# Optimization experiments

Measured on AMD Instinct MI355X. Metric: run time of the kernel, lower is better.

Reference implementation:

```python
import jax, jax.numpy as jnp
import numpy as np


def _hard_sigmoid(x):
    # Keras ConvLSTM2D default recurrent_activation
    return jnp.clip(0.2 * x + 0.5, 0.0, 1.0)


def _conv_same(x, w):
    # x: [B,H,W,Cin], w: [kh,kw,Cin,Cout]
    return jax.lax.conv_general_dilated(
        x, w, window_strides=(1, 1), padding='SAME',
        dimension_numbers=('NHWC', 'HWIO', 'NHWC'))


def setup_inputs() -> dict:
    key = jax.random.key(0)
    ks = jax.random.split(key, 6)
    B, T, H, W, F = 16, 16, 64, 64, 64
    return {
        'inputs': jax.random.normal(ks[0], (B, T, H, W, 1), jnp.float32),  # only T is used
        'h0': jax.random.normal(ks[1], (B, H, W, F), jnp.float32),
        'c0': jax.random.normal(ks[2], (B, H, W, F), jnp.float32),
        'kernels': jax.random.normal(ks[3], (T, 3, 3, F, 4 * F), jnp.float32) * 0.05,
        'rec_kernels': jax.random.normal(ks[4], (T, 3, 3, F, 4 * F), jnp.float32) * 0.05,
        'bias': jnp.zeros((T, 4 * F), jnp.float32),
    }


def reference(inputs, h0, c0, kernels, rec_kernels, bias):
    # The layer feeds h back as the cell input each step, so the cell input x == h.
    # By linearity, conv(h, Wk) + conv(h, Uk) == conv(h, Wk + Uk); we fuse the two convs.
    # Gate order (Keras ConvLSTM2DCell): i, f, c, o.
    def step(carry, params):
        h, c = carry
        Wk, Uk, b = params  # [3,3,F,4F], [3,3,F,4F], [4F]
        z = _conv_same(h, Wk + Uk) + b  # [B,H,W,4F]
        zi, zf, zc, zo = jnp.split(z, 4, axis=-1)
        i = _hard_sigmoid(zi)
        f = _hard_sigmoid(zf)
        c_new = f * c + i * jnp.tanh(zc)
        o = _hard_sigmoid(zo)
        h_new = o * jnp.tanh(c_new)
        return (h_new, c_new), h_new

    (_, _), hs = jax.lax.scan(step, (h0, c0), (kernels, rec_kernels, bias))
    return jnp.moveaxis(hs, 0, 1)  # [B, T, H, W, F]
```

## Files before the change

### kernel.cpp

```cpp
#include <hip/hip_runtime.h>
#include <math.h>

typedef _Float16 f16;
typedef _Float16 f16x4 __attribute__((ext_vector_type(4)));
typedef _Float16 f16x8 __attribute__((ext_vector_type(8)));
typedef float f32x4 __attribute__((ext_vector_type(4)));

#define NB 16
#define NT 16
#define NH 64
#define NW 64
#define NF 64
#define NG 256
#define HWF ((size_t)NH * NW * NF)
#define OUT_BSTRIDE ((size_t)NT * HWF)
#define RS2 8448
#define ZS 258
#define WSTEP ((size_t)18432)

#define MFMA(a, b, c) __builtin_amdgcn_mfma_f32_16x16x32_f16((a), (b), (c), 0, 0, 0)

__device__ __forceinline__ void gload_lds16(const void* g, void* l) {
    __builtin_amdgcn_global_load_lds(
        (const __attribute__((address_space(1))) unsigned int*)(g),
        (__attribute__((address_space(3))) unsigned int*)(l), 16, 0, 0);
}

__device__ __forceinline__ float hsig(float x) {
    return fminf(fmaxf(0.2f * x + 0.5f, 0.0f), 1.0f);
}

__device__ __forceinline__ float ftanh(float x) {
    float t = __builtin_amdgcn_exp2f(x * 2.885390081777927f);
    return 1.0f - 2.0f * __builtin_amdgcn_rcpf(t + 1.0f);
}

__global__ void fuse_w_hi(const float* __restrict__ k, const float* __restrict__ rk,
                          f16* __restrict__ wf2) {
    int idx = blockIdx.x * 256 + threadIdx.x;
    if (idx >= NT * 9 * NG * 8) return;
    int g8   = idx & 7;
    int cout = (idx >> 3) & 255;
    int tt   = idx >> 11;
    int tap  = tt % 9;
    int t    = tt / 9;
    int kk = g8 >> 2, lg = g8 & 3;

    const float* ks = k  + (size_t)tt * NF * NG + cout;
    const float* rs = rk + (size_t)tt * NF * NG + cout;

    f16 hi8[8];
#pragma unroll
    for (int j = 0; j < 8; ++j) {
        int cin = kk * 32 + lg * 8 + j;
        hi8[j] = (f16)(ks[(size_t)cin * NG] + rs[(size_t)cin * NG]);
    }
    const int lane = lg * 16 + (cout & 15);
    size_t chunk = (size_t)t * WSTEP + (size_t)(tap * 2 + kk) * 1024 +
                   (size_t)(cout >> 4) * 64 + lane;
    *(f16x8*)&wf2[chunk * 8] = *(f16x8*)hi8;
}

__global__ void f32_to_f16(const float* __restrict__ src, f16* __restrict__ dst, int n4) {
    int i = blockIdx.x * 256 + threadIdx.x;
    if (i >= n4) return;
    float4 v = ((const float4*)src)[i];
    f16x4 o = { (f16)v.x, (f16)v.y, (f16)v.z, (f16)v.w };
    *(f16x4*)&dst[(size_t)i * 4] = o;
}

__global__ void __launch_bounds__(512, 4)
convlstm_mfma_step(const f16* __restrict__ h2in, f16* __restrict__ h2out,
                   f16* __restrict__ cbuf,
                   float* __restrict__ hout,
                   const f16* __restrict__ wt,
                   const float* __restrict__ bias)
{
    __shared__ __align__(16) unsigned char lds[67584];

    const int tid  = threadIdx.x;
    const int w    = tid >> 6;
    const int lane = tid & 63;

    const int id    = blockIdx.x;
    const int bb    = ((id & 7) << 1) + ((id >> 8) & 1);
    const int y0    = ((id >> 3) & 31) * 2;

    if (tid < 64) {
        int row = tid >> 4, side = (tid >> 3) & 1, j = tid & 7;
        *(f16x8*)&lds[row * RS2 + side * (65 * 128) + j * 16] = (f16x8)(_Float16)0.0f;
    }

    {
        const int r    = w >> 1;
        const int gy   = y0 - 1 + r;
        const int half = w & 1;
        const unsigned dbase = r * RS2 + 128 + half * 4096;
        if (gy >= 0 && gy < NH) {
            const unsigned char* gsrc = (const unsigned char*)h2in +
                ((((size_t)bb * NH + gy) * NW) << 7);
#pragma unroll
            for (int i = 0; i < 4; ++i) {
                const int xrel = half * 32 + i * 8 + (lane >> 3);
                const unsigned src = ((unsigned)xrel << 7) +
                    ((unsigned)((lane & 7) ^ ((xrel + 1) & 7)) << 4);
                gload_lds16(gsrc + src, (void*)&lds[dbase + i * 1024]);
            }
        } else {
            const f16x8 zf = (f16x8)(_Float16)0.0f;
#pragma unroll
            for (int i = 0; i < 4; ++i)
                *(f16x8*)&lds[dbase + i * 1024 + lane * 16] = zf;
        }
    }
    __syncthreads();

    const int wm = w >> 2;
    const int wn = w & 3;
    const int lm = lane & 15;
    const int lg = lane >> 4;

    f32x4 acc[4][4];
#pragma unroll
    for (int mf = 0; mf < 4; ++mf)
#pragma unroll
        for (int nf = 0; nf < 4; ++nf) acc[mf][nf] = (f32x4)0.0f;

    unsigned av[3][2];
#pragma unroll
    for (int d = 0; d < 3; ++d)
#pragma unroll
        for (int kk = 0; kk < 2; ++kk) {
            const int tx = lm + d;
            av[d][kk] = (unsigned)(tx * 128 +
                        (((kk * 4 + lg) ^ (tx & 7)) << 4));
        }

    const f16x8* wb = (const f16x8*)wt + (size_t)(wn * 4) * 64 + lane;

    f16x8 bh[4];
#pragma unroll
    for (int it = 0; it < 18; ++it) {
        const int tap = it >> 1, kk = it & 1;
#pragma unroll
        for (int nf = 0; nf < 4; ++nf)
            bh[nf] = wb[(size_t)it * 1024 + nf * 64];
        const int ty = tap / 3;
        const int d  = tap - ty * 3;
        const unsigned abase = (unsigned)((wm + ty) * RS2) + av[d][kk];
        __builtin_amdgcn_s_setprio(1);
#pragma unroll
        for (int mf = 0; mf < 4; ++mf) {
            const f16x8 ah = *(const f16x8*)&lds[abase + mf * 2048];
#pragma unroll
            for (int nf = 0; nf < 4; ++nf)
                acc[mf][nf] = MFMA(ah, bh[nf], acc[mf][nf]);
        }
        __builtin_amdgcn_s_setprio(0);
    }

    __syncthreads();

    float* zbuf = (float*)lds;
    const int f = tid & 63;
    const float bi = bias[f], bfv = bias[64 + f], bcv = bias[128 + f], bov = bias[192 + f];

#pragma unroll 1
    for (int half = 0; half < 2; ++half) {
        if (wm == half) {
#pragma unroll
            for (int mf = 0; mf < 4; ++mf)
#pragma unroll
                for (int nf = 0; nf < 4; ++nf)
#pragma unroll
                    for (int j = 0; j < 4; ++j)
                        zbuf[(mf * 16 + lg * 4 + j) * ZS + wn * 64 + nf * 16 + lm] =
                            acc[mf][nf][j];
        }
        __syncthreads();
        const int gy = y0 + half;
#pragma unroll 1
        for (int k2 = 0; k2 < 8; ++k2) {
            const int x = (tid >> 6) + k2 * 8;
            const float* zz = zbuf + x * ZS;
            float zi  = zz[f]       + bi;
            float zfv = zz[64 + f]  + bfv;
            float zc  = zz[128 + f] + bcv;
            float zo  = zz[192 + f] + bov;
            size_t goff = (((size_t)bb * NH + gy) * NW + x) * NF + f;
            float cp = (float)cbuf[goff];
            float ig = hsig(zi), fg = hsig(zfv), og = hsig(zo);
            float cn = fg * cp + ig * ftanh(zc);
            cbuf[goff] = (f16)cn;
            float hn = og * ftanh(cn);
            hout[(size_t)bb * OUT_BSTRIDE + (((size_t)gy * NW + x) * NF + f)] = hn;
            h2out[goff] = (f16)hn;
        }
        __syncthreads();
    }
}

extern "C" void kernel_launch(void* const* d_in, const int* in_sizes, int n_in,
                              void* d_out, int out_size, void* d_ws, size_t ws_size,
                              hipStream_t stream) {
    const float* h0    = (const float*)d_in[1];
    const float* c0    = (const float*)d_in[2];
    const float* kern  = (const float*)d_in[3];
    const float* rkern = (const float*)d_in[4];
    const float* bias  = (const float*)d_in[5];
    float* out = (float*)d_out;

    f16* wf2   = (f16*)d_ws;
    f16* h2a   = wf2 + (size_t)NT * WSTEP * 8;
    f16* h2b   = h2a + (size_t)NB * HWF;
    f16* cbuf  = h2b + (size_t)NB * HWF;

    const int n4 = (int)(NB * HWF / 4);
    fuse_w_hi<<<(NT * 9 * NG * 8 + 255) / 256, 256, 0, stream>>>(kern, rkern, wf2);
    f32_to_f16<<<(n4 + 255) / 256, 256, 0, stream>>>(h0, h2a, n4);
    f32_to_f16<<<(n4 + 255) / 256, 256, 0, stream>>>(c0, cbuf, n4);

    for (int t = 0; t < NT; ++t) {
        const f16* hin = (t & 1) ? h2b : h2a;
        f16* hnx       = (t & 1) ? h2a : h2b;
        convlstm_mfma_step<<<dim3(512), 512, 0, stream>>>(
            hin, hnx, cbuf,
            out + (size_t)t * HWF,
            wf2 + (size_t)t * WSTEP * 8,
            bias + t * NG);
    }
}
```

Before: 444.0 us.

## Permute weight columns so each wave holds all four gates, drop LDS epilogue

Reorders the fused weight layout so the four N-fragments a wave computes correspond to the i, f, c, o gates of the same 16 features. The LSTM gate math can then run directly on MFMA accumulators in registers, which removes the LDS staging of the z tile, the extra barriers and the shrunken-but-large shared buffer. The first weight fragment load is also hoisted above the h tile load to overlap latency. Global stores become less coalesced (16 features per row segment instead of 64), and the smaller LDS footprint may allow higher occupancy.

```diff
diff --git a/kernel.cpp b/kernel.cpp
--- a/kernel.cpp
+++ b/kernel.cpp
@@ -15,7 +15,6 @@
 #define HWF ((size_t)NH * NW * NF)
 #define OUT_BSTRIDE ((size_t)NT * HWF)
 #define RS2 8448
-#define ZS 258
 #define WSTEP ((size_t)18432)
 
 #define MFMA(a, b, c) __builtin_amdgcn_mfma_f32_16x16x32_f16((a), (b), (c), 0, 0, 0)
@@ -56,8 +55,9 @@
         hi8[j] = (f16)(ks[(size_t)cin * NG] + rs[(size_t)cin * NG]);
     }
     const int lane = lg * 16 + (cout & 15);
+    const int cb   = ((cout >> 4) & 3) * 4 + (cout >> 6);
     size_t chunk = (size_t)t * WSTEP + (size_t)(tap * 2 + kk) * 1024 +
-                   (size_t)(cout >> 4) * 64 + lane;
+                   (size_t)cb * 64 + lane;
     *(f16x8*)&wf2[chunk * 8] = *(f16x8*)hi8;
 }
 
@@ -76,15 +76,26 @@
                    const f16* __restrict__ wt,
                    const float* __restrict__ bias)
 {
-    __shared__ __align__(16) unsigned char lds[67584];
+    __shared__ __align__(16) unsigned char lds[4 * RS2];
 
     const int tid  = threadIdx.x;
     const int w    = tid >> 6;
     const int lane = tid & 63;
 
-    const int id    = blockIdx.x;
-    const int bb    = ((id & 7) << 1) + ((id >> 8) & 1);
-    const int y0    = ((id >> 3) & 31) * 2;
+    const int id = blockIdx.x;
+    const int bb = ((id & 7) << 1) + ((id >> 8) & 1);
+    const int y0 = ((id >> 3) & 31) * 2;
+
+    const int wm = w >> 2;
+    const int wn = w & 3;
+    const int lm = lane & 15;
+    const int lg = lane >> 4;
+
+    const f16x8* wb = (const f16x8*)wt + (size_t)(wn * 4) * 64 + lane;
+    f16x8 bh[4];
+#pragma unroll
+    for (int nf = 0; nf < 4; ++nf)
+        bh[nf] = wb[nf * 64];
 
     if (tid < 64) {
         int row = tid >> 4, side = (tid >> 3) & 1, j = tid & 7;
@@ -115,11 +126,6 @@
     }
     __syncthreads();
 
-    const int wm = w >> 2;
-    const int wn = w & 3;
-    const int lm = lane & 15;
-    const int lg = lane >> 4;
-
     f32x4 acc[4][4];
 #pragma unroll
     for (int mf = 0; mf < 4; ++mf)
@@ -136,15 +142,14 @@
                         (((kk * 4 + lg) ^ (tx & 7)) << 4));
         }
 
-    const f16x8* wb = (const f16x8*)wt + (size_t)(wn * 4) * 64 + lane;
-
-    f16x8 bh[4];
 #pragma unroll
     for (int it = 0; it < 18; ++it) {
+        if (it > 0) {
+#pragma unroll
+            for (int nf = 0; nf < 4; ++nf)
+                bh[nf] = wb[(size_t)it * 1024 + nf * 64];
+        }
         const int tap = it >> 1, kk = it & 1;
-#pragma unroll
-        for (int nf = 0; nf < 4; ++nf)
-            bh[nf] = wb[(size_t)it * 1024 + nf * 64];
         const int ty = tap / 3;
         const int d  = tap - ty * 3;
         const unsigned abase = (unsigned)((wm + ty) * RS2) + av[d][kk];
@@ -159,44 +164,31 @@
         __builtin_amdgcn_s_setprio(0);
     }
 
-    __syncthreads();
-
-    float* zbuf = (float*)lds;
-    const int f = tid & 63;
-    const float bi = bias[f], bfv = bias[64 + f], bcv = bias[128 + f], bov = bias[192 + f];
-
-#pragma unroll 1
-    for (int half = 0; half < 2; ++half) {
-        if (wm == half) {
-#pragma unroll
-            for (int mf = 0; mf < 4; ++mf)
-#pragma unroll
-                for (int nf = 0; nf < 4; ++nf)
-#pragma unroll
-                    for (int j = 0; j < 4; ++j)
-                        zbuf[(mf * 16 + lg * 4 + j) * ZS + wn * 64 + nf * 16 + lm] =
-                            acc[mf][nf][j];
-        }
-        __syncthreads();
-        const int gy = y0 + half;
-#pragma unroll 1
-        for (int k2 = 0; k2 < 8; ++k2) {
-            const int x = (tid >> 6) + k2 * 8;
-            const float* zz = zbuf + x * ZS;
-            float zi  = zz[f]       + bi;
-            float zfv = zz[64 + f]  + bfv;
-            float zc  = zz[128 + f] + bcv;
-            float zo  = zz[192 + f] + bov;
-            size_t goff = (((size_t)bb * NH + gy) * NW + x) * NF + f;
-            float cp = (float)cbuf[goff];
-            float ig = hsig(zi), fg = hsig(zfv), og = hsig(zo);
-            float cn = fg * cp + ig * ftanh(zc);
-            cbuf[goff] = (f16)cn;
-            float hn = og * ftanh(cn);
-            hout[(size_t)bb * OUT_BSTRIDE + (((size_t)gy * NW + x) * NF + f)] = hn;
-            h2out[goff] = (f16)hn;
-        }
-        __syncthreads();
+    const int f  = wn * 16 + lm;
+    const int gy = y0 + wm;
+    const float b0 = bias[f], b1 = bias[64 + f], b2 = bias[128 + f], b3 = bias[192 + f];
+
+#pragma unroll
+    for (int mf = 0; mf < 4; ++mf) {
+        const int xb = mf * 16 + lg * 4;
+        const size_t base = ((((size_t)bb * NH + gy) * NW + xb) << 6) + f;
+        f16 cp4[4];
+#pragma unroll
+        for (int j = 0; j < 4; ++j)
+            cp4[j] = cbuf[base + (size_t)j * 64];
+#pragma unroll
+        for (int j = 0; j < 4; ++j) {
+            const float zi  = acc[mf][0][j] + b0;
+            const float zfv = acc[mf][1][j] + b1;
+            const float zc  = acc[mf][2][j] + b2;
+            const float zo  = acc[mf][3][j] + b3;
+            const float ig = hsig(zi), fg = hsig(zfv), og = hsig(zo);
+            const float cn = fg * (float)cp4[j] + ig * ftanh(zc);
+            cbuf[base + (size_t)j * 64] = (f16)cn;
+            const float hn = og * ftanh(cn);
+            hout[(size_t)bb * OUT_BSTRIDE + (((size_t)gy * NW + xb + j) << 6) + f] = hn;
+            h2out[base + (size_t)j * 64] = (f16)hn;
+        }
     }
 }
 
```

After: 384.3 us. -13.4%, faster.
